# Kernel tuning notes

Hardware: AMD Instinct MI355X
Metric: run time of the kernel (lower is better)

Reference implementation:

```python
import jax, jax.numpy as jnp
import numpy as np

B, C, T_TEXT, T_FEAT = 16, 256, 512, 4096
DELTA = 0.1  # temperature


def setup_inputs() -> dict:
    key = jax.random.key(0)
    k1, k2 = jax.random.split(key)
    x = jax.random.normal(k1, (B, C, T_TEXT), dtype=jnp.float32)
    # durations: avg ~8 frames per token so cumsum spans ~T_FEAT frames
    w = jax.random.uniform(k2, (B, T_TEXT), dtype=jnp.float32) * 16.0
    x_mask = jnp.ones((B, T_FEAT), dtype=bool)   # frame-level mask (B, T_feat)
    y_mask = jnp.ones((B, T_TEXT), dtype=bool)   # token-level mask (B, T_text)
    return {"x": x, "w": w, "x_mask": x_mask, "y_mask": y_mask}


def reference(x, w, x_mask, y_mask):
    # x: (B, C, T_text), w: (B, T_text)
    t_feat = x_mask.shape[-1]
    # frame time grid, masked frames zeroed as in reference impl
    t = jnp.arange(t_feat, dtype=x.dtype)[None, :] * x_mask.astype(x.dtype)  # (B, T_feat)
    # Gaussian centers per token: cumulative duration minus half of own duration
    c = jnp.cumsum(w, axis=-1) - 0.5 * w  # (B, T_text)
    # energy: -delta * (t - c)^2  -> (B, T_feat, T_text)
    energy = -DELTA * jnp.square(t[:, :, None] - c[:, None, :])
    energy = jnp.where(y_mask[:, None, :], energy, -jnp.inf)
    attn = jax.nn.softmax(energy, axis=-1)  # softmax over tokens (T_text)
    # weighted sum over tokens: (B, T_feat, T_text) x (B, C, T_text) -> (B, C, T_feat)
    return jnp.einsum('bft,bct->bcf', attn, x)
```

## Files before the change

### kernel.cpp

```cpp
#include <hip/hip_runtime.h>
#include <math.h>


constexpr int BB  = 16;
constexpr int CC  = 256;
constexpr int TT  = 512;
constexpr int TF  = 4096;
constexpr float DEL = 0.1f;

constexpr int TILE_F = 32;
constexpr int MAXW   = 32;
constexpr int MAXN   = 64;
constexpr float CUT  = 200.0f;

constexpr int NTILE = TF / TILE_F * BB;
constexpr size_t WS_CW = (size_t)BB * TT * 4;

typedef __attribute__((ext_vector_type(8))) short short8v;
typedef __attribute__((ext_vector_type(4))) float f32x4v;

__device__ __forceinline__ unsigned cvtpk(float lo, float hi) {
  unsigned r;
  asm("v_cvt_pk_bf16_f32 %0, %1, %2" : "=v"(r) : "v"(lo), "v"(hi));
  return r;
}

__device__ __forceinline__ void tile_map(int lin, int& b, int& f0) {
  const int xcd  = lin & 7;
  const int slot = lin >> 3;
  b  = xcd * 2 + (slot >> 7);
  f0 = (slot & 127) * TILE_F;
}

__global__ __launch_bounds__(256)
void prep_k(const float* __restrict__ w, float* __restrict__ cw,
            ushort4* __restrict__ win) {
  __shared__ float sc[TT];
  const int b = blockIdx.x, tid = threadIdx.x;

  if (tid < 64) {
    const int l = tid;
    const float* wr = w + b * TT + l * 8;
    float v[8];
    *(float4*)&v[0] = *(const float4*)&wr[0];
    *(float4*)&v[4] = *(const float4*)&wr[4];
    double s[8]; double run = 0.0;
#pragma unroll
    for (int k = 0; k < 8; ++k) { run += (double)v[k]; s[k] = run; }
    double tot = run;
    for (int off = 1; off < 64; off <<= 1) {
      double o = __shfl_up(tot, off, 64);
      if (l >= off) tot += o;
    }
    const double base = tot - run;
    float c8[8];
#pragma unroll
    for (int k = 0; k < 8; ++k) c8[k] = (float)(base + s[k] - 0.5 * (double)v[k]);
#pragma unroll
    for (int k = 0; k < 8; ++k) sc[l * 8 + k] = c8[k];
    if (blockIdx.y == 0) {
      float* co = cw + b * TT + l * 8;
#pragma unroll
      for (int k = 0; k < 8; ++k) co[k] = c8[k];
    }
  }
  __syncthreads();

  const int f = blockIdx.y * 256 + tid;
  const float fv = (float)f;
  int lb = 0, h = TT;
  while (lb < h) { int m = (lb + h) >> 1; if (sc[m] < fv) lb = m + 1; else h = m; }
  int js = (lb < TT) ? lb : TT - 1;
  float dmin = fabsf(sc[js] - fv);
  if (lb > 0) { float d = fabsf(sc[lb - 1] - fv); if (d <= dmin) { dmin = d; js = lb - 1; } }
  const float D = sqrtf(fmaf(dmin, dmin, CUT));
  int lo = 0; h = TT;
  { const float lv = fv - D;
    while (lo < h) { int m = (lo + h) >> 1; if (sc[m] < lv) lo = m + 1; else h = m; } }
  int hi = lo; h = TT;
  { const float hv = fv + D;
    while (hi < h) { int m = (hi + h) >> 1; if (sc[m] <= hv) hi = m + 1; else h = m; } }
  if (hi - lo > MAXW) {
    int nl = js - MAXW / 2; if (nl < lo) nl = lo;
    lo = nl;
    if (hi > lo + MAXW) hi = lo + MAXW;
  }
  win[b * TF + f] = make_ushort4((unsigned short)js, (unsigned short)lo,
                                 (unsigned short)hi, 0);
}

__global__ __launch_bounds__(256, 4)
void gauss_up(const float* __restrict__ x, const float* __restrict__ cw,
              const ushort4* __restrict__ win, float* __restrict__ out) {
  __shared__ __align__(16) unsigned short xs[CC * MAXN];
  __shared__ __align__(16) unsigned short pb2[TILE_F * MAXN];
  __shared__ int s_lo4;

  int b, f0; tile_map(blockIdx.x, b, f0);
  const int tid = threadIdx.x;
  const float* cwb = cw + b * TT;

  int js = 0, n = 0, LO4 = 0;
  float fv = 0.f;
  if (tid < TILE_F) {
    const ushort4 wv = win[b * TF + f0 + tid];
    js = wv.x;
    int LO = wv.y, HI = wv.z;
    fv = (float)(f0 + tid);
#pragma unroll
    for (int m = 16; m >= 1; m >>= 1) {
      LO = min(LO, __shfl_xor(LO, m, 32));
      HI = max(HI, __shfl_xor(HI, m, 32));
    }
    LO4 = LO & ~3;
    if (HI - LO4 > MAXN) {
      const int js0  = __shfl(js, 0, 32);
      const int js31 = __shfl(js, 31, 32);
      int nl = (((js0 + js31) >> 1) - MAXN / 2) & ~3;
      if (nl < LO4) nl = LO4;
      LO4 = nl;
    }
    if (LO4 > TT - MAXN) LO4 = TT - MAXN;
    if (HI > LO4 + MAXN) HI = LO4 + MAXN;
    n = HI - LO4;
    if (tid == 0) s_lo4 = LO4;
  }
  __syncthreads();
  LO4 = s_lo4;

  if (tid < TILE_F) {
    const float dmin = fabsf(fv - cwb[js]);
    const float m0 = DEL * dmin * dmin;
    float e[MAXN];
    float Z = 0.f;
#pragma unroll
    for (int jc = 0; jc < MAXN / 4; ++jc) {
      const float4 c4 = *(const float4*)(cwb + LO4 + 4 * jc);
      const int jb = 4 * jc;
      float d0 = fv - c4.x, d1 = fv - c4.y, d2 = fv - c4.z, d3 = fv - c4.w;
      float e0 = __expf(fmaf(-DEL, d0 * d0, m0));
      float e1 = __expf(fmaf(-DEL, d1 * d1, m0));
      float e2 = __expf(fmaf(-DEL, d2 * d2, m0));
      float e3 = __expf(fmaf(-DEL, d3 * d3, m0));
      e0 = (jb + 0 < n) ? e0 : 0.f;
      e1 = (jb + 1 < n) ? e1 : 0.f;
      e2 = (jb + 2 < n) ? e2 : 0.f;
      e3 = (jb + 3 < n) ? e3 : 0.f;
      e[jb + 0] = e0; e[jb + 1] = e1; e[jb + 2] = e2; e[jb + 3] = e3;
      Z += (e0 + e1) + (e2 + e3);
    }
    const float rz = 1.f / fmaxf(Z, 1e-30f);
    const int rsw = (tid & 7) << 4;
#pragma unroll
    for (int jc = 0; jc < MAXN / 4; ++jc) {
      const unsigned q0 = cvtpk(e[4 * jc + 0] * rz, e[4 * jc + 1] * rz);
      const unsigned q1 = cvtpk(e[4 * jc + 2] * rz, e[4 * jc + 3] * rz);
      *(uint2*)((char*)pb2 + tid * 128 + ((jc * 8) ^ rsw)) = make_uint2(q0, q1);
    }
  } else {
    const float* xb = x + (size_t)b * CC * TT + LO4;
    for (int u = tid - 32; u < CC * 8; u += 224) {
      const int r  = u >> 3;
      const int cq = (u & 7) * 2;
      const float* rp = xb + (size_t)r * TT + cq * 4;
      const float4 a  = *(const float4*)rp;
      const float4 bv = *(const float4*)(rp + 4);
      uint4 q;
      q.x = cvtpk(a.x, a.y);  q.y = cvtpk(a.z, a.w);
      q.z = cvtpk(bv.x, bv.y); q.w = cvtpk(bv.z, bv.w);
      *(uint4*)((char*)xs + r * 128 + ((cq * 8) ^ ((r & 7) << 4))) = q;
    }
  }
  __syncthreads();

  const int wv   = tid >> 6;
  const int lane = tid & 63;
  const int cbase = wv * 64;
  const int l15 = lane & 15, lq = lane >> 4;

  f32x4v acc[4][2];
#pragma unroll
  for (int mt = 0; mt < 4; ++mt)
#pragma unroll
    for (int nt = 0; nt < 2; ++nt) acc[mt][nt] = (f32x4v){0.f, 0.f, 0.f, 0.f};

  short8v bfr[2][2];
#pragma unroll
  for (int nt = 0; nt < 2; ++nt)
#pragma unroll
    for (int ks = 0; ks < 2; ++ks) {
      const int row = nt * 16 + l15;
      const int col = (ks * 64 + lq * 16) ^ ((row & 7) << 4);
      bfr[nt][ks] = *(const short8v*)((const char*)pb2 + row * 128 + col);
    }

#pragma unroll
  for (int mt = 0; mt < 4; ++mt) {
    const int row = cbase + mt * 16 + l15;
    const int sw  = (row & 7) << 4;
    const short8v a0 = *(const short8v*)((const char*)xs + row * 128 + ((lq * 16) ^ sw));
    const short8v a1 = *(const short8v*)((const char*)xs + row * 128 + ((64 + lq * 16) ^ sw));
#pragma unroll
    for (int nt = 0; nt < 2; ++nt) {
      acc[mt][nt] = __builtin_amdgcn_mfma_f32_16x16x32_bf16(a0, bfr[nt][0], acc[mt][nt], 0, 0, 0);
      acc[mt][nt] = __builtin_amdgcn_mfma_f32_16x16x32_bf16(a1, bfr[nt][1], acc[mt][nt], 0, 0, 0);
    }
  }

  float* ob = out + ((size_t)b * CC + cbase + lq * 4) * TF + f0 + l15;
#pragma unroll
  for (int mt = 0; mt < 4; ++mt)
#pragma unroll
    for (int nt = 0; nt < 2; ++nt) {
#pragma unroll
      for (int reg = 0; reg < 4; ++reg)
        ob[(size_t)(mt * 16 + reg) * TF + nt * 16] = acc[mt][nt][reg];
    }
}

extern "C" void kernel_launch(void* const* d_in, const int* in_sizes, int n_in,
                              void* d_out, int out_size, void* d_ws, size_t ws_size,
                              hipStream_t stream) {
  const float* x = (const float*)d_in[0];
  const float* w = (const float*)d_in[1];
  float* out = (float*)d_out;

  float*   cw = (float*)d_ws;
  ushort4* wn = (ushort4*)((char*)d_ws + WS_CW);

  prep_k  <<<dim3(BB, TF / 256), dim3(256), 0, stream>>>(w, cw, wn);
  gauss_up<<<dim3(NTILE),        dim3(256), 0, stream>>>(x, cw, wn, out);
}
```

Measured before the change: 97.21 us.

## Precompute softmax weights in prep kernel and stage full x rows per block

The prep kernel now computes the softmax weights for each 32-frame tile, writes them to workspace as bf16, and records a per-tile window start. The main kernel is restructured so that each block loads a 64-channel by full-token slice of x into LDS once and reuses it across 16 frame tiles (512 frames), instead of reloading an x window for every 32-frame tile. This removes repeated x reads and conversions, and takes the exp work out of the MFMA kernel. In exchange it adds a global round trip for the weight matrix, uses 64KB of LDS with fewer resident blocks, and holds many accumulators in registers.

```diff
diff --git a/kernel.cpp b/kernel.cpp
--- a/kernel.cpp
+++ b/kernel.cpp
@@ -14,7 +14,7 @@
 constexpr float CUT  = 200.0f;
 
 constexpr int NTILE = TF / TILE_F * BB;
-constexpr size_t WS_CW = (size_t)BB * TT * 4;
+constexpr size_t WS_META = 16384;
 
 typedef __attribute__((ext_vector_type(8))) short short8v;
 typedef __attribute__((ext_vector_type(4))) float f32x4v;
@@ -25,16 +25,9 @@
   return r;
 }
 
-__device__ __forceinline__ void tile_map(int lin, int& b, int& f0) {
-  const int xcd  = lin & 7;
-  const int slot = lin >> 3;
-  b  = xcd * 2 + (slot >> 7);
-  f0 = (slot & 127) * TILE_F;
-}
-
 __global__ __launch_bounds__(256)
-void prep_k(const float* __restrict__ w, float* __restrict__ cw,
-            ushort4* __restrict__ win) {
+void prep2(const float* __restrict__ w, unsigned short* __restrict__ P,
+           int* __restrict__ meta) {
   __shared__ float sc[TT];
   const int b = blockIdx.x, tid = threadIdx.x;
 
@@ -53,16 +46,9 @@
       if (l >= off) tot += o;
     }
     const double base = tot - run;
-    float c8[8];
-#pragma unroll
-    for (int k = 0; k < 8; ++k) c8[k] = (float)(base + s[k] - 0.5 * (double)v[k]);
-#pragma unroll
-    for (int k = 0; k < 8; ++k) sc[l * 8 + k] = c8[k];
-    if (blockIdx.y == 0) {
-      float* co = cw + b * TT + l * 8;
-#pragma unroll
-      for (int k = 0; k < 8; ++k) co[k] = c8[k];
-    }
+#pragma unroll
+    for (int k = 0; k < 8; ++k)
+      sc[l * 8 + k] = (float)(base + s[k] - 0.5 * (double)v[k]);
   }
   __syncthreads();
 
@@ -85,137 +71,134 @@
     lo = nl;
     if (hi > lo + MAXW) hi = lo + MAXW;
   }
-  win[b * TF + f] = make_ushort4((unsigned short)js, (unsigned short)lo,
-                                 (unsigned short)hi, 0);
-}
-
-__global__ __launch_bounds__(256, 4)
-void gauss_up(const float* __restrict__ x, const float* __restrict__ cw,
-              const ushort4* __restrict__ win, float* __restrict__ out) {
-  __shared__ __align__(16) unsigned short xs[CC * MAXN];
-  __shared__ __align__(16) unsigned short pb2[TILE_F * MAXN];
-  __shared__ int s_lo4;
-
-  int b, f0; tile_map(blockIdx.x, b, f0);
+
+  int LO = lo, HI = hi;
+#pragma unroll
+  for (int m = 16; m >= 1; m >>= 1) {
+    LO = min(LO, __shfl_xor(LO, m, 32));
+    HI = max(HI, __shfl_xor(HI, m, 32));
+  }
+  int LO8 = LO & ~7;
+  if (HI - LO8 > MAXN) {
+    const int js0  = __shfl(js, 0, 32);
+    const int js31 = __shfl(js, 31, 32);
+    int nl = (((js0 + js31) >> 1) - MAXN / 2) & ~7;
+    if (nl < LO8) nl = LO8;
+    LO8 = nl;
+  }
+  if (LO8 > TT - MAXN) LO8 = TT - MAXN;
+  if (LO8 < 0) LO8 = 0;
+  int n = HI - LO8;
+  if (n > MAXN) n = MAXN;
+  if (n < 1) n = 1;
+
+  const float m0 = DEL * dmin * dmin;
+  float e[MAXN];
+  float Z = 0.f;
+#pragma unroll
+  for (int jc = 0; jc < MAXN / 4; ++jc) {
+    const float4 c4 = *(const float4*)&sc[LO8 + 4 * jc];
+    const int jb = 4 * jc;
+    float d0 = fv - c4.x, d1 = fv - c4.y, d2 = fv - c4.z, d3 = fv - c4.w;
+    float e0 = __expf(fmaf(-DEL, d0 * d0, m0));
+    float e1 = __expf(fmaf(-DEL, d1 * d1, m0));
+    float e2 = __expf(fmaf(-DEL, d2 * d2, m0));
+    float e3 = __expf(fmaf(-DEL, d3 * d3, m0));
+    e0 = (jb + 0 < n) ? e0 : 0.f;
+    e1 = (jb + 1 < n) ? e1 : 0.f;
+    e2 = (jb + 2 < n) ? e2 : 0.f;
+    e3 = (jb + 3 < n) ? e3 : 0.f;
+    e[jb + 0] = e0; e[jb + 1] = e1; e[jb + 2] = e2; e[jb + 3] = e3;
+    Z += (e0 + e1) + (e2 + e3);
+  }
+  const float rz = 1.f / fmaxf(Z, 1e-30f);
+
+  const int gt   = b * (TF / TILE_F) + blockIdx.y * 8 + (tid >> 5);
+  const int lane = tid & 31;
+  unsigned short* pt = P + (size_t)gt * (TILE_F * MAXN) + lane * MAXN;
+#pragma unroll
+  for (int jc = 0; jc < MAXN / 8; ++jc) {
+    uint4 q;
+    q.x = cvtpk(e[8 * jc + 0] * rz, e[8 * jc + 1] * rz);
+    q.y = cvtpk(e[8 * jc + 2] * rz, e[8 * jc + 3] * rz);
+    q.z = cvtpk(e[8 * jc + 4] * rz, e[8 * jc + 5] * rz);
+    q.w = cvtpk(e[8 * jc + 6] * rz, e[8 * jc + 7] * rz);
+    *(uint4*)(pt + 8 * jc) = q;
+  }
+  if (lane == 0) meta[gt] = LO8;
+}
+
+__global__ __launch_bounds__(256, 2)
+void gauss3(const float* __restrict__ x, const unsigned short* __restrict__ P,
+            const int* __restrict__ meta, float* __restrict__ out) {
+  __shared__ __align__(16) unsigned short xs[64 * TT];
+
+  const int lin = blockIdx.x;
+  const int xcd = lin & 7;
+  const int r   = lin >> 3;
+  const int b   = xcd * 2 + (r & 1);
+  const int cg  = (r >> 1) & 3;
+  const int seg = r >> 3;
+  const int ch0 = cg * 64;
+  const int f0  = seg * 512;
   const int tid = threadIdx.x;
-  const float* cwb = cw + b * TT;
-
-  int js = 0, n = 0, LO4 = 0;
-  float fv = 0.f;
-  if (tid < TILE_F) {
-    const ushort4 wv = win[b * TF + f0 + tid];
-    js = wv.x;
-    int LO = wv.y, HI = wv.z;
-    fv = (float)(f0 + tid);
-#pragma unroll
-    for (int m = 16; m >= 1; m >>= 1) {
-      LO = min(LO, __shfl_xor(LO, m, 32));
-      HI = max(HI, __shfl_xor(HI, m, 32));
+
+  for (int u = tid; u < 64 * 64; u += 256) {
+    const int row = u >> 6, chunk = u & 63;
+    const float* rp = x + ((size_t)b * CC + ch0 + row) * TT + chunk * 8;
+    const float4 a  = *(const float4*)rp;
+    const float4 bv = *(const float4*)(rp + 4);
+    uint4 q;
+    q.x = cvtpk(a.x, a.y);   q.y = cvtpk(a.z, a.w);
+    q.z = cvtpk(bv.x, bv.y); q.w = cvtpk(bv.z, bv.w);
+    *(uint4*)((char*)xs + row * 1024 + ((chunk * 16) ^ ((row & 7) << 4))) = q;
+  }
+  __syncthreads();
+
+  const int wv = tid >> 6, lane = tid & 63;
+  const int l15 = lane & 15, lq = lane >> 4;
+  const int gtb = b * (TF / TILE_F) + seg * 16;
+
+  int lo8s[16];
+#pragma unroll
+  for (int t = 0; t < 16; ++t) lo8s[t] = meta[gtb + t];
+
+  f32x4v acc[16][2];
+#pragma unroll
+  for (int t = 0; t < 16; ++t)
+#pragma unroll
+    for (int nt = 0; nt < 2; ++nt) acc[t][nt] = (f32x4v){0.f, 0.f, 0.f, 0.f};
+
+  const int arow = wv * 16 + l15;
+  const int sw   = (arow & 7) << 4;
+
+#pragma unroll
+  for (int t = 0; t < 16; ++t) {
+    const char* pt = (const char*)(P + (size_t)(gtb + t) * (TILE_F * MAXN));
+    short8v bfr[2][2];
+#pragma unroll
+    for (int nt = 0; nt < 2; ++nt)
+#pragma unroll
+      for (int ks = 0; ks < 2; ++ks)
+        bfr[nt][ks] = *(const short8v*)(pt + (nt * 16 + l15) * 128 + ks * 64 + lq * 16);
+    const int cb = lo8s[t] * 2;
+    const short8v a0 = *(const short8v*)((const char*)xs + arow * 1024 + ((cb + lq * 16) ^ sw));
+    const short8v a1 = *(const short8v*)((const char*)xs + arow * 1024 + ((cb + 64 + lq * 16) ^ sw));
+#pragma unroll
+    for (int nt = 0; nt < 2; ++nt) {
+      acc[t][nt] = __builtin_amdgcn_mfma_f32_16x16x32_bf16(a0, bfr[nt][0], acc[t][nt], 0, 0, 0);
+      acc[t][nt] = __builtin_amdgcn_mfma_f32_16x16x32_bf16(a1, bfr[nt][1], acc[t][nt], 0, 0, 0);
     }
-    LO4 = LO & ~3;
-    if (HI - LO4 > MAXN) {
-      const int js0  = __shfl(js, 0, 32);
-      const int js31 = __shfl(js, 31, 32);
-      int nl = (((js0 + js31) >> 1) - MAXN / 2) & ~3;
-      if (nl < LO4) nl = LO4;
-      LO4 = nl;
-    }
-    if (LO4 > TT - MAXN) LO4 = TT - MAXN;
-    if (HI > LO4 + MAXN) HI = LO4 + MAXN;
-    n = HI - LO4;
-    if (tid == 0) s_lo4 = LO4;
-  }
-  __syncthreads();
-  LO4 = s_lo4;
-
-  if (tid < TILE_F) {
-    const float dmin = fabsf(fv - cwb[js]);
-    const float m0 = DEL * dmin * dmin;
-    float e[MAXN];
-    float Z = 0.f;
-#pragma unroll
-    for (int jc = 0; jc < MAXN / 4; ++jc) {
-      const float4 c4 = *(const float4*)(cwb + LO4 + 4 * jc);
-      const int jb = 4 * jc;
-      float d0 = fv - c4.x, d1 = fv - c4.y, d2 = fv - c4.z, d3 = fv - c4.w;
-      float e0 = __expf(fmaf(-DEL, d0 * d0, m0));
-      float e1 = __expf(fmaf(-DEL, d1 * d1, m0));
-      float e2 = __expf(fmaf(-DEL, d2 * d2, m0));
-      float e3 = __expf(fmaf(-DEL, d3 * d3, m0));
-      e0 = (jb + 0 < n) ? e0 : 0.f;
-      e1 = (jb + 1 < n) ? e1 : 0.f;
-      e2 = (jb + 2 < n) ? e2 : 0.f;
-      e3 = (jb + 3 < n) ? e3 : 0.f;
-      e[jb + 0] = e0; e[jb + 1] = e1; e[jb + 2] = e2; e[jb + 3] = e3;
-      Z += (e0 + e1) + (e2 + e3);
-    }
-    const float rz = 1.f / fmaxf(Z, 1e-30f);
-    const int rsw = (tid & 7) << 4;
-#pragma unroll
-    for (int jc = 0; jc < MAXN / 4; ++jc) {
-      const unsigned q0 = cvtpk(e[4 * jc + 0] * rz, e[4 * jc + 1] * rz);
-      const unsigned q1 = cvtpk(e[4 * jc + 2] * rz, e[4 * jc + 3] * rz);
-      *(uint2*)((char*)pb2 + tid * 128 + ((jc * 8) ^ rsw)) = make_uint2(q0, q1);
-    }
-  } else {
-    const float* xb = x + (size_t)b * CC * TT + LO4;
-    for (int u = tid - 32; u < CC * 8; u += 224) {
-      const int r  = u >> 3;
-      const int cq = (u & 7) * 2;
-      const float* rp = xb + (size_t)r * TT + cq * 4;
-      const float4 a  = *(const float4*)rp;
-      const float4 bv = *(const float4*)(rp + 4);
-      uint4 q;
-      q.x = cvtpk(a.x, a.y);  q.y = cvtpk(a.z, a.w);
-      q.z = cvtpk(bv.x, bv.y); q.w = cvtpk(bv.z, bv.w);
-      *(uint4*)((char*)xs + r * 128 + ((cq * 8) ^ ((r & 7) << 4))) = q;
-    }
-  }
-  __syncthreads();
-
-  const int wv   = tid >> 6;
-  const int lane = tid & 63;
-  const int cbase = wv * 64;
-  const int l15 = lane & 15, lq = lane >> 4;
-
-  f32x4v acc[4][2];
-#pragma unroll
-  for (int mt = 0; mt < 4; ++mt)
-#pragma unroll
-    for (int nt = 0; nt < 2; ++nt) acc[mt][nt] = (f32x4v){0.f, 0.f, 0.f, 0.f};
-
-  short8v bfr[2][2];
-#pragma unroll
-  for (int nt = 0; nt < 2; ++nt)
-#pragma unroll
-    for (int ks = 0; ks < 2; ++ks) {
-      const int row = nt * 16 + l15;
-      const int col = (ks * 64 + lq * 16) ^ ((row & 7) << 4);
-      bfr[nt][ks] = *(const short8v*)((const char*)pb2 + row * 128 + col);
-    }
-
-#pragma unroll
-  for (int mt = 0; mt < 4; ++mt) {
-    const int row = cbase + mt * 16 + l15;
-    const int sw  = (row & 7) << 4;
-    const short8v a0 = *(const short8v*)((const char*)xs + row * 128 + ((lq * 16) ^ sw));
-    const short8v a1 = *(const short8v*)((const char*)xs + row * 128 + ((64 + lq * 16) ^ sw));
-#pragma unroll
-    for (int nt = 0; nt < 2; ++nt) {
-      acc[mt][nt] = __builtin_amdgcn_mfma_f32_16x16x32_bf16(a0, bfr[nt][0], acc[mt][nt], 0, 0, 0);
-      acc[mt][nt] = __builtin_amdgcn_mfma_f32_16x16x32_bf16(a1, bfr[nt][1], acc[mt][nt], 0, 0, 0);
-    }
-  }
-
-  float* ob = out + ((size_t)b * CC + cbase + lq * 4) * TF + f0 + l15;
-#pragma unroll
-  for (int mt = 0; mt < 4; ++mt)
-#pragma unroll
-    for (int nt = 0; nt < 2; ++nt) {
-#pragma unroll
-      for (int reg = 0; reg < 4; ++reg)
-        ob[(size_t)(mt * 16 + reg) * TF + nt * 16] = acc[mt][nt][reg];
-    }
+  }
+
+  float* ob = out + ((size_t)b * CC + ch0 + wv * 16 + lq * 4) * TF + f0 + l15;
+#pragma unroll
+  for (int reg = 0; reg < 4; ++reg)
+#pragma unroll
+    for (int t = 0; t < 16; ++t)
+#pragma unroll
+      for (int nt = 0; nt < 2; ++nt)
+        ob[(size_t)reg * TF + t * 32 + nt * 16] = acc[t][nt][reg];
 }
 
 extern "C" void kernel_launch(void* const* d_in, const int* in_sizes, int n_in,
@@ -225,9 +208,9 @@
   const float* w = (const float*)d_in[1];
   float* out = (float*)d_out;
 
-  float*   cw = (float*)d_ws;
-  ushort4* wn = (ushort4*)((char*)d_ws + WS_CW);
-
-  prep_k  <<<dim3(BB, TF / 256), dim3(256), 0, stream>>>(w, cw, wn);
-  gauss_up<<<dim3(NTILE),        dim3(256), 0, stream>>>(x, cw, wn, out);
-}
+  int*            meta = (int*)d_ws;
+  unsigned short* P    = (unsigned short*)((char*)d_ws + WS_META);
+
+  prep2 <<<dim3(BB, TF / 256), dim3(256), 0, stream>>>(w, P, meta);
+  gauss3<<<dim3(512),          dim3(256), 0, stream>>>(x, P, meta, out);
+}
```

Measured after the change: 108.8 us. 11.9% more time.
